# Performance work log

Hardware: AMD Instinct MI355X
Metric: run time of the kernel (lower is better)

Reference implementation:

```python
import jax, jax.numpy as jnp
import numpy as np

N = 100000
E = 1600000
D_IN = 256
N_HEADS = 4
OUT_SZ = 32  # output_dim // n_heads = 128 // 4
ALPHA = 0.2  # leaky relu slope


def setup_inputs() -> dict:
    key = jax.random.key(0)
    ks = jax.random.split(key, 8)
    x = jax.random.normal(ks[0], (N, D_IN), dtype=jnp.float32)
    edge_row = jax.random.randint(ks[1], (E,), 0, N, dtype=jnp.int32)
    edge_col = jax.random.randint(ks[2], (E,), 0, N, dtype=jnp.int32)
    # per-head params: W (conv1d k=1, no bias), a1/a2 (conv1d k=1 with bias)
    W = jax.random.normal(ks[3], (N_HEADS, D_IN, OUT_SZ), dtype=jnp.float32) * (1.0 / np.sqrt(D_IN))
    a1 = jax.random.normal(ks[4], (N_HEADS, OUT_SZ), dtype=jnp.float32) * (1.0 / np.sqrt(OUT_SZ))
    b1 = jnp.zeros((N_HEADS,), dtype=jnp.float32)
    a2 = jax.random.normal(ks[5], (N_HEADS, OUT_SZ), dtype=jnp.float32) * (1.0 / np.sqrt(OUT_SZ))
    b2 = jnp.zeros((N_HEADS,), dtype=jnp.float32)
    return {"x": x, "W": W, "a1": a1, "b1": b1, "a2": a2, "b2": b2,
            "edge_row": edge_row, "edge_col": edge_col}


def _gat_heads(x, W, a1, b1, a2, b2, edge_row, edge_col):
    # per-head linear transform: [H, N, O]
    fts = jnp.einsum('nd,hdo->hno', x, W)
    f1 = jnp.einsum('hno,ho->hn', fts, a1) + b1[:, None]  # [H, N]
    f2 = jnp.einsum('hno,ho->hn', fts, a2) + b2[:, None]  # [H, N]
    # edge logits: f1[row] + f2[col]  (adj values are 1)
    logits = f1[:, edge_row] + f2[:, edge_col]            # [H, E]
    lr = jnp.maximum(ALPHA * logits, logits)
    # segment softmax over each node's incoming edge set (rows)
    seg_max = jax.vmap(lambda v: jax.ops.segment_max(v, edge_row, num_segments=N))(lr)
    ex = jnp.exp(lr - seg_max[:, edge_row])
    denom = jax.vmap(lambda v: jax.ops.segment_sum(v, edge_row, num_segments=N))(ex)
    coef = ex / denom[:, edge_row]                        # [H, E]
    # SpMM aggregation: out[h, i] = sum_{e: row(e)=i} coef[h,e] * fts[h, col(e)]
    msg = coef[:, :, None] * fts[:, edge_col, :]          # [H, E, O]
    agg = jax.vmap(lambda m: jax.ops.segment_sum(m, edge_row, num_segments=N))(msg)  # [H, N, O]
    h = jnp.transpose(agg, (1, 0, 2)).reshape(N, N_HEADS * OUT_SZ)  # concat heads
    return jax.nn.elu(h)[None]  # [1, N, output_dim]


def reference(x, W, a1, b1, a2, b2, edge_row, edge_col):
    return _gat_heads(x, W, a1, b1, a2, b2, edge_row, edge_col)
```

## Files before the change

### kernel.cpp

```cpp
#include <hip/hip_runtime.h>
#include <hip/hip_bf16.h>
#include <math.h>

#define ALPHA 0.2f
#define PB_EDGES 4096
#define MAXT 256

typedef __attribute__((ext_vector_type(8))) short short8;
typedef __attribute__((ext_vector_type(4))) float floatx4;

__device__ __forceinline__ ushort f2bf(float f) {
    uint u = __float_as_uint(f);
    u += 0x7fff + ((u >> 16) & 1);
    return (ushort)(u >> 16);
}

__device__ __forceinline__ short8 pack8(float4 lo, float4 hi) {
    short8 r;
    r[0] = (short)f2bf(lo.x); r[1] = (short)f2bf(lo.y);
    r[2] = (short)f2bf(lo.z); r[3] = (short)f2bf(lo.w);
    r[4] = (short)f2bf(hi.x); r[5] = (short)f2bf(hi.y);
    r[6] = (short)f2bf(hi.z); r[7] = (short)f2bf(hi.w);
    return r;
}

__global__ __launch_bounds__(256) void k_wprep(const float* __restrict__ W,
                                               ushort* __restrict__ Wt)
{
    int g = blockIdx.x * 256 + threadIdx.x;
    int c = g >> 8, d = g & 255;
    Wt[g] = f2bf(W[(c >> 5) * 8192 + d * 32 + (c & 31)]);
}

__global__ __launch_bounds__(256) void k_gemm(const float* __restrict__ x,
                                              const ushort* __restrict__ Wt,
                                              const float* __restrict__ a1v,
                                              const float* __restrict__ b1v,
                                              const float* __restrict__ a2v,
                                              const float* __restrict__ b2v,
                                              ushort* __restrict__ fts2,
                                              float* __restrict__ f1,
                                              float* __restrict__ f2, int M)
{
    __shared__ __align__(16) ushort smem[32768];
    const int t  = threadIdx.x;
    const int m0 = blockIdx.x * 128;

#pragma unroll
    for (int i = 0; i < 16; i++) {
        int f = i * 256 + t;
        int lane_ = f & 63, ksct = f >> 6;
        int ks = ksct & 7, ct = ksct >> 3;
        int mm = lane_ & 15, qq = lane_ >> 4;
        *(uint4*)&smem[f * 8] = *(const uint4*)&Wt[(ct * 16 + mm) * 256 + ks * 32 + qq * 8];
    }

    const int w = t >> 6, lane = t & 63;
    const int mm = lane & 15, qq = lane >> 4;

    int row0 = m0 + w * 32 + mm;
    int row1 = row0 + 16;
    int r0c = (row0 < M) ? row0 : (M - 1);
    int r1c = (row1 < M) ? row1 : (M - 1);
    const float* ar0 = x + (size_t)r0c * 256 + qq * 8;
    const float* ar1 = x + (size_t)r1c * 256 + qq * 8;
    short8 afrag[2][8];
#pragma unroll
    for (int ks = 0; ks < 8; ks++) {
        float4 lo0 = *(const float4*)(ar0 + ks * 32);
        float4 hi0 = *(const float4*)(ar0 + ks * 32 + 4);
        float4 lo1 = *(const float4*)(ar1 + ks * 32);
        float4 hi1 = *(const float4*)(ar1 + ks * 32 + 4);
        afrag[0][ks] = pack8(lo0, hi0);
        afrag[1][ks] = pack8(lo1, hi1);
    }

    floatx4 acc[2][8];
#pragma unroll
    for (int r = 0; r < 2; r++)
#pragma unroll
        for (int ct = 0; ct < 8; ct++) acc[r][ct] = (floatx4){0.f, 0.f, 0.f, 0.f};

    __syncthreads();

#pragma unroll
    for (int ks = 0; ks < 8; ks++) {
#pragma unroll
        for (int ct = 0; ct < 8; ct++) {
            short8 b8 = *(const short8*)&smem[((ct * 8 + ks) * 64 + lane) * 8];
            acc[0][ct] = __builtin_amdgcn_mfma_f32_16x16x32_bf16(afrag[0][ks], b8, acc[0][ct], 0, 0, 0);
            acc[1][ct] = __builtin_amdgcn_mfma_f32_16x16x32_bf16(afrag[1][ks], b8, acc[1][ct], 0, 0, 0);
        }
    }

    __syncthreads();
    ushort* ftsL = smem;
#pragma unroll
    for (int r = 0; r < 2; r++)
#pragma unroll
        for (int ct = 0; ct < 8; ct++)
#pragma unroll
            for (int i = 0; i < 4; i++) {
                int rowl = w * 32 + r * 16 + qq * 4 + i;
                ftsL[rowl * 136 + ct * 16 + mm] = f2bf(acc[r][ct][i]);
            }
    __syncthreads();

    {
        int rowl = t >> 1, half = t & 1;
        int gr = m0 + rowl;
        if (gr < M) {
            const uint4* src = (const uint4*)&ftsL[rowl * 136 + half * 64];
            uint4* dst = (uint4*)(fts2 + (size_t)gr * 128 + half * 64);
#pragma unroll
            for (int i = 0; i < 8; i++) dst[i] = src[i];
        }
    }
#pragma unroll
    for (int p = 0; p < 2; p++) {
        int task = p * 256 + t;
        int rowl = task >> 2, h = task & 3;
        int gr = m0 + rowl;
        if (gr < M) {
            const ushort* fr = &ftsL[rowl * 136 + h * 32];
            float s1 = 0.f, s2 = 0.f;
#pragma unroll
            for (int o = 0; o < 32; o++) {
                float v = __uint_as_float((uint)fr[o] << 16);
                s1 = fmaf(v, a1v[h * 32 + o], s1);
                s2 = fmaf(v, a2v[h * 32 + o], s2);
            }
            f1[gr * 4 + h] = s1 + b1v[h];
            f2[gr * 4 + h] = s2 + b2v[h];
        }
    }
}

__global__ __launch_bounds__(256) void k_phist(const int* __restrict__ erow,
                                               int* __restrict__ bcnt, int E, int NB)
{
    __shared__ int h[512];
    for (int i = threadIdx.x; i < 512; i += 256) h[i] = 0;
    __syncthreads();
    int b0 = blockIdx.x * PB_EDGES;
    int bend = b0 + PB_EDGES; if (bend > E) bend = E;
    for (int j = b0 + threadIdx.x; j < bend; j += 256)
        atomicAdd(&h[erow[j] >> 8], 1);
    __syncthreads();
    for (int i = threadIdx.x; i < NB; i += 256)
        if (h[i]) atomicAdd(&bcnt[i], h[i]);
}

__global__ __launch_bounds__(256) void k_scan_buckets(const int* __restrict__ bcnt,
                                                      int* __restrict__ base,
                                                      int* __restrict__ bcursor,
                                                      int NB, int E)
{
    __shared__ int s[256];
    int t = threadIdx.x;
    int i0 = 2 * t, i1 = 2 * t + 1;
    int v0 = (i0 < NB) ? bcnt[i0] : 0;
    int v1 = (i1 < NB) ? bcnt[i1] : 0;
    int tsum = v0 + v1;
    s[t] = tsum;
    __syncthreads();
    for (int off = 1; off < 256; off <<= 1) {
        int u = (t >= off) ? s[t - off] : 0;
        __syncthreads();
        s[t] += u;
        __syncthreads();
    }
    int excl = s[t] - tsum;
    if (i0 < NB) { base[i0] = excl;      bcursor[i0] = excl; }
    if (i1 < NB) { base[i1] = excl + v0; bcursor[i1] = excl + v0; }
    if (t == 0) base[NB] = E;
}

__global__ __launch_bounds__(256) void k_pscatter(const int* __restrict__ erow,
                                                  const int* __restrict__ ecol,
                                                  int* __restrict__ bcursor,
                                                  uint* __restrict__ part, int E)
{
    __shared__ int h[512];
    __shared__ int cur[512];
    for (int i = threadIdx.x; i < 512; i += 256) h[i] = 0;
    __syncthreads();
    int b0 = blockIdx.x * PB_EDGES;
    int bend = b0 + PB_EDGES; if (bend > E) bend = E;
    for (int j = b0 + threadIdx.x; j < bend; j += 256)
        atomicAdd(&h[erow[j] >> 8], 1);
    __syncthreads();
    for (int i = threadIdx.x; i < 512; i += 256)
        cur[i] = h[i] ? atomicAdd(&bcursor[i], h[i]) : 0;
    __syncthreads();
    for (int j = b0 + threadIdx.x; j < bend; j += 256) {
        int r = erow[j], c = ecol[j];
        int p = atomicAdd(&cur[r >> 8], 1);
        part[p] = ((uint)(r & 255) << 24) | (uint)c;
    }
}

__global__ __launch_bounds__(256) void k_bucket(const uint* __restrict__ part,
                                                const int* __restrict__ base,
                                                int* __restrict__ row_start,
                                                int* __restrict__ col_sorted,
                                                int Nn, int NB, int E)
{
    __shared__ int cnt[256];
    __shared__ int s[256];
    __shared__ int cur[256];
    const int b = blockIdx.x, t = threadIdx.x;
    const int start = base[b], end = base[b + 1];

    cnt[t] = 0;
    __syncthreads();
    for (int j = start + t; j < end; j += 256)
        atomicAdd(&cnt[part[j] >> 24], 1);
    __syncthreads();
    int v = cnt[t];
    s[t] = v;
    __syncthreads();
    for (int off = 1; off < 256; off <<= 1) {
        int u = (t >= off) ? s[t - off] : 0;
        __syncthreads();
        s[t] += u;
        __syncthreads();
    }
    int excl = s[t] - v;
    int r = b * 256 + t;
    if (r < Nn) row_start[r] = start + excl;
    if (b == 0 && t == 0) row_start[Nn] = E;
    cur[t] = start + excl;
    __syncthreads();
    for (int j = start + t; j < end; j += 256) {
        uint rc = part[j];
        int p = atomicAdd(&cur[rc >> 24], 1);
        col_sorted[p] = (int)(rc & 0xffffffu);
    }
}

__global__ __launch_bounds__(256) void k_gat_row(const ushort* __restrict__ fts2,
                                                 const float4* __restrict__ f1,
                                                 const float4* __restrict__ f2,
                                                 const int* __restrict__ row_start,
                                                 const int* __restrict__ cols,
                                                 float* __restrict__ out, int Nn)
{
    __shared__ __align__(16) float eLs[4][MAXT * 4];
    __shared__ uint vLs[4][MAXT];

    const int wid  = threadIdx.x >> 6;
    const int lane = threadIdx.x & 63;
    const int slot = lane >> 4;
    const int sub  = lane & 15;
    const int hsel = sub >> 2;

    const int rbase = (blockIdx.x * 4 + wid) * 4;
    if (rbase >= Nn) return;

    const int myr = rbase + slot;
    const bool rowAct = (myr < Nn);
    const int i0 = rowAct ? myr : Nn;
    const int i1 = (myr + 1 < Nn) ? (myr + 1) : Nn;
    const int sB = row_start[i0];
    const int eB = row_start[i1];
    const int degTot = eB - sB;

    const int s0 = __shfl(sB, 0, 64);
    const int b1 = __shfl(sB, 16, 64);
    const int b2 = __shfl(sB, 32, 64);
    const int b3 = __shfl(sB, 48, 64);
    const int T  = __shfl(eB, 48, 64) - s0;

    float ds = 0.f;
    float acc[8];
#pragma unroll
    for (int i = 0; i < 8; i++) acc[i] = 0.f;

    const char* ftsB = (const char*)fts2;
    const uint  laneOff = (uint)sub * 16;
    float* eLw = eLs[wid];
    uint*  vLw = vLs[wid];

    for (int base = 0; base < T; base += MAXT) {
        int tc = T - base; if (tc > MAXT) tc = MAXT;
        int tcPad = (tc + 63) & ~63;

        for (int lt = lane; lt < tcPad; lt += 64) {
            bool act = (lt < tc);
            int j = s0 + base + lt;
            int c = act ? cols[j] : 0;
            int rsel = (j >= b1) + (j >= b2) + (j >= b3);
            int fi = rbase + rsel; if (fi >= Nn) fi = Nn - 1;
            float4 f1r = f1[fi];
            float4 f2v = f2[c];
            float l0 = f1r.x + f2v.x; l0 = fmaxf(l0, ALPHA * l0);
            float l1 = f1r.y + f2v.y; l1 = fmaxf(l1, ALPHA * l1);
            float l2 = f1r.z + f2v.z; l2 = fmaxf(l2, ALPHA * l2);
            float l3 = f1r.w + f2v.w; l3 = fmaxf(l3, ALPHA * l3);
            float e0 = act ? __expf(l0) : 0.f;
            float e1 = act ? __expf(l1) : 0.f;
            float e2 = act ? __expf(l2) : 0.f;
            float e3 = act ? __expf(l3) : 0.f;
            asm volatile("s_waitcnt lgkmcnt(0)" ::: "memory");
            *(float4*)&eLw[lt * 4] = make_float4(e0, e1, e2, e3);
            vLw[lt] = (uint)c << 8;
        }
        asm volatile("s_waitcnt lgkmcnt(0)" ::: "memory");

        int lo = sB - s0 - base; lo = (lo < 0) ? 0 : ((lo > tc) ? tc : lo);
        int hi = eB - s0 - base; hi = (hi < 0) ? 0 : ((hi > tc) ? tc : hi);
        int ni = hi - lo;
        int eIdx = lo * 4 + hsel;
#pragma unroll 4
        for (int g = 0; g < ni; g++) {
            float ee = eLw[eIdx + g * 4];
            uint  vo = vLw[lo + g] + laneOff;
            uint4 vv = *(const uint4*)(ftsB + vo);
            ds += ee;
            float ve;
            ve = __uint_as_float(vv.x << 16);          acc[0] = fmaf(ee, ve, acc[0]);
            ve = __uint_as_float(vv.x & 0xffff0000u);  acc[1] = fmaf(ee, ve, acc[1]);
            ve = __uint_as_float(vv.y << 16);          acc[2] = fmaf(ee, ve, acc[2]);
            ve = __uint_as_float(vv.y & 0xffff0000u);  acc[3] = fmaf(ee, ve, acc[3]);
            ve = __uint_as_float(vv.z << 16);          acc[4] = fmaf(ee, ve, acc[4]);
            ve = __uint_as_float(vv.z & 0xffff0000u);  acc[5] = fmaf(ee, ve, acc[5]);
            ve = __uint_as_float(vv.w << 16);          acc[6] = fmaf(ee, ve, acc[6]);
            ve = __uint_as_float(vv.w & 0xffff0000u);  acc[7] = fmaf(ee, ve, acc[7]);
        }
    }

    float dsel = (degTot > 0) ? ds : 1.f;
    float rinv = 1.0f / dsel;
    float o[8];
#pragma unroll
    for (int i = 0; i < 8; i++) {
        float v = acc[i] * rinv;
        o[i] = (v > 0.f) ? v : (__expf(v) - 1.0f);
    }
    if (rowAct) {
        float4* dst = (float4*)(out + (size_t)myr * 128 + sub * 8);
        dst[0] = make_float4(o[0], o[1], o[2], o[3]);
        dst[1] = make_float4(o[4], o[5], o[6], o[7]);
    }
}

extern "C" void kernel_launch(void* const* d_in, const int* in_sizes, int n_in,
                              void* d_out, int out_size, void* d_ws, size_t ws_size,
                              hipStream_t stream)
{
    const float* x   = (const float*)d_in[0];
    const float* W   = (const float*)d_in[1];
    const float* a1  = (const float*)d_in[2];
    const float* b1  = (const float*)d_in[3];
    const float* a2  = (const float*)d_in[4];
    const float* b2  = (const float*)d_in[5];
    const int*   erow = (const int*)d_in[6];
    const int*   ecol = (const int*)d_in[7];
    float* out = (float*)d_out;

    const int N = in_sizes[0] / 256;
    const int E = in_sizes[6];
    const int NB = (N + 255) >> 8;

    char*  ws  = (char*)d_ws;
    size_t off = 0;
    auto carve = [&](size_t bytes) -> char* {
        char* p = ws + off;
        off += (bytes + 255) & ~(size_t)255;
        return p;
    };
    ushort* fts2      = (ushort*)carve((size_t)N * 128 * 2);
    ushort* Wt        = (ushort*)carve((size_t)128 * 256 * 2);
    float*  f1        = (float*)carve((size_t)N * 4 * 4);
    float*  f2        = (float*)carve((size_t)N * 4 * 4);
    int*    row_start = (int*)carve(((size_t)N + 1) * 4);
    int*    bcnt      = (int*)carve(512 * 4);
    int*    base      = (int*)carve(513 * 4);
    int*    bcursor   = (int*)carve(512 * 4);
    int*    col_sorted= (int*)carve((size_t)E * 4);
    uint*   part      = (uint*)carve((size_t)E * 4);
    (void)ws_size;

    k_wprep<<<128, 256, 0, stream>>>(W, Wt);
    k_gemm<<<(N + 127) / 128, 256, 0, stream>>>(x, Wt, a1, b1, a2, b2, fts2, f1, f2, N);

    hipMemsetAsync(bcnt, 0, 512 * 4, stream);
    int npb = (E + PB_EDGES - 1) / PB_EDGES;
    k_phist<<<npb, 256, 0, stream>>>(erow, bcnt, E, NB);
    k_scan_buckets<<<1, 256, 0, stream>>>(bcnt, base, bcursor, NB, E);
    k_pscatter<<<npb, 256, 0, stream>>>(erow, ecol, bcursor, part, E);
    k_bucket<<<NB, 256, 0, stream>>>(part, base, row_start, col_sorted, N, NB, E);

    k_gat_row<<<(N + 15) / 16, 256, 0, stream>>>(fts2, (const float4*)f1, (const float4*)f2,
                                                 row_start, col_sorted, out, N);
}
```

Baseline: 337.3 us.

## Software-pipeline SpMM gathers with dual accumulators; read pre-swizzled W directly in GEMM

The aggregation loop now processes two edges per iteration into separate accumulators and prefetches the next pair's feature gathers and weights before doing the current FMAs. This hides gather latency and breaks the dependency chain on one accumulator. The weight prep kernel now writes W in the MFMA fragment layout, so the GEMM loads B fragments straight from global/L2 and no longer stages W in shared memory, which drops two barriers and a 64KB LDS buffer. MAXT is halved to shrink the per-wave LDS staging chunks. Register pressure goes up and the edge staging loop runs more iterations.

```diff
diff --git a/kernel.cpp b/kernel.cpp
--- a/kernel.cpp
+++ b/kernel.cpp
@@ -4,7 +4,7 @@
 
 #define ALPHA 0.2f
 #define PB_EDGES 4096
-#define MAXT 256
+#define MAXT 128
 
 typedef __attribute__((ext_vector_type(8))) short short8;
 typedef __attribute__((ext_vector_type(4))) float floatx4;
@@ -24,11 +24,28 @@
     return r;
 }
 
+__device__ __forceinline__ void fma8(float* acc, float e, uint4 v) {
+    acc[0] = fmaf(e, __uint_as_float(v.x << 16),         acc[0]);
+    acc[1] = fmaf(e, __uint_as_float(v.x & 0xffff0000u), acc[1]);
+    acc[2] = fmaf(e, __uint_as_float(v.y << 16),         acc[2]);
+    acc[3] = fmaf(e, __uint_as_float(v.y & 0xffff0000u), acc[3]);
+    acc[4] = fmaf(e, __uint_as_float(v.z << 16),         acc[4]);
+    acc[5] = fmaf(e, __uint_as_float(v.z & 0xffff0000u), acc[5]);
+    acc[6] = fmaf(e, __uint_as_float(v.w << 16),         acc[6]);
+    acc[7] = fmaf(e, __uint_as_float(v.w & 0xffff0000u), acc[7]);
+}
+
 __global__ __launch_bounds__(256) void k_wprep(const float* __restrict__ W,
                                                ushort* __restrict__ Wt)
 {
     int g = blockIdx.x * 256 + threadIdx.x;
-    int c = g >> 8, d = g & 255;
+    int u = g & 7;
+    int lane = (g >> 3) & 63;
+    int ksct = g >> 9;
+    int ks = ksct & 7, ct = ksct >> 3;
+    int mm = lane & 15, qq = lane >> 4;
+    int c = ct * 16 + mm;
+    int d = ks * 32 + qq * 8 + u;
     Wt[g] = f2bf(W[(c >> 5) * 8192 + d * 32 + (c & 31)]);
 }
 
@@ -42,18 +59,9 @@
                                               float* __restrict__ f1,
                                               float* __restrict__ f2, int M)
 {
-    __shared__ __align__(16) ushort smem[32768];
+    __shared__ __align__(16) ushort ftsL[128 * 136];
     const int t  = threadIdx.x;
     const int m0 = blockIdx.x * 128;
-
-#pragma unroll
-    for (int i = 0; i < 16; i++) {
-        int f = i * 256 + t;
-        int lane_ = f & 63, ksct = f >> 6;
-        int ks = ksct & 7, ct = ksct >> 3;
-        int mm = lane_ & 15, qq = lane_ >> 4;
-        *(uint4*)&smem[f * 8] = *(const uint4*)&Wt[(ct * 16 + mm) * 256 + ks * 32 + qq * 8];
-    }
 
     const int w = t >> 6, lane = t & 63;
     const int mm = lane & 15, qq = lane >> 4;
@@ -81,20 +89,17 @@
 #pragma unroll
         for (int ct = 0; ct < 8; ct++) acc[r][ct] = (floatx4){0.f, 0.f, 0.f, 0.f};
 
-    __syncthreads();
-
+    const ushort* Wf = Wt + (size_t)lane * 8;
 #pragma unroll
     for (int ks = 0; ks < 8; ks++) {
 #pragma unroll
         for (int ct = 0; ct < 8; ct++) {
-            short8 b8 = *(const short8*)&smem[((ct * 8 + ks) * 64 + lane) * 8];
+            short8 b8 = *(const short8*)&Wf[(ct * 8 + ks) * 64 * 8];
             acc[0][ct] = __builtin_amdgcn_mfma_f32_16x16x32_bf16(afrag[0][ks], b8, acc[0][ct], 0, 0, 0);
             acc[1][ct] = __builtin_amdgcn_mfma_f32_16x16x32_bf16(afrag[1][ks], b8, acc[1][ct], 0, 0, 0);
         }
     }
 
-    __syncthreads();
-    ushort* ftsL = smem;
 #pragma unroll
     for (int r = 0; r < 2; r++)
 #pragma unroll
@@ -272,10 +277,10 @@
     const int b3 = __shfl(sB, 48, 64);
     const int T  = __shfl(eB, 48, 64) - s0;
 
-    float ds = 0.f;
-    float acc[8];
-#pragma unroll
-    for (int i = 0; i < 8; i++) acc[i] = 0.f;
+    float dsA = 0.f, dsB = 0.f;
+    float accA[8], accB[8];
+#pragma unroll
+    for (int i = 0; i < 8; i++) { accA[i] = 0.f; accB[i] = 0.f; }
 
     const char* ftsB = (const char*)fts2;
     const uint  laneOff = (uint)sub * 16;
@@ -310,32 +315,48 @@
 
         int lo = sB - s0 - base; lo = (lo < 0) ? 0 : ((lo > tc) ? tc : lo);
         int hi = eB - s0 - base; hi = (hi < 0) ? 0 : ((hi > tc) ? tc : hi);
-        int ni = hi - lo;
-        int eIdx = lo * 4 + hsel;
-#pragma unroll 4
-        for (int g = 0; g < ni; g++) {
-            float ee = eLw[eIdx + g * 4];
-            uint  vo = vLw[lo + g] + laneOff;
-            uint4 vv = *(const uint4*)(ftsB + vo);
-            ds += ee;
-            float ve;
-            ve = __uint_as_float(vv.x << 16);          acc[0] = fmaf(ee, ve, acc[0]);
-            ve = __uint_as_float(vv.x & 0xffff0000u);  acc[1] = fmaf(ee, ve, acc[1]);
-            ve = __uint_as_float(vv.y << 16);          acc[2] = fmaf(ee, ve, acc[2]);
-            ve = __uint_as_float(vv.y & 0xffff0000u);  acc[3] = fmaf(ee, ve, acc[3]);
-            ve = __uint_as_float(vv.z << 16);          acc[4] = fmaf(ee, ve, acc[4]);
-            ve = __uint_as_float(vv.z & 0xffff0000u);  acc[5] = fmaf(ee, ve, acc[5]);
-            ve = __uint_as_float(vv.w << 16);          acc[6] = fmaf(ee, ve, acc[6]);
-            ve = __uint_as_float(vv.w & 0xffff0000u);  acc[7] = fmaf(ee, ve, acc[7]);
-        }
-    }
-
+        int g = lo;
+
+        float eA0 = 0.f, eB0 = 0.f;
+        uint4 vA0 = make_uint4(0, 0, 0, 0), vB0 = make_uint4(0, 0, 0, 0);
+        if (g + 1 < hi) {
+            eA0 = eLw[g * 4 + hsel];
+            eB0 = eLw[g * 4 + 4 + hsel];
+            vA0 = *(const uint4*)(ftsB + (vLw[g] + laneOff));
+            vB0 = *(const uint4*)(ftsB + (vLw[g + 1] + laneOff));
+        }
+#pragma unroll 2
+        for (; g + 3 < hi; g += 2) {
+            float eA1 = eLw[(g + 2) * 4 + hsel];
+            float eB1 = eLw[(g + 2) * 4 + 4 + hsel];
+            uint4 vA1 = *(const uint4*)(ftsB + (vLw[g + 2] + laneOff));
+            uint4 vB1 = *(const uint4*)(ftsB + (vLw[g + 3] + laneOff));
+            dsA += eA0; dsB += eB0;
+            fma8(accA, eA0, vA0);
+            fma8(accB, eB0, vB0);
+            eA0 = eA1; eB0 = eB1; vA0 = vA1; vB0 = vB1;
+        }
+        if (g + 1 < hi) {
+            dsA += eA0; dsB += eB0;
+            fma8(accA, eA0, vA0);
+            fma8(accB, eB0, vB0);
+            g += 2;
+        }
+        if (g < hi) {
+            float eA = eLw[g * 4 + hsel];
+            uint4 vA = *(const uint4*)(ftsB + (vLw[g] + laneOff));
+            dsA += eA;
+            fma8(accA, eA, vA);
+        }
+    }
+
+    float ds = dsA + dsB;
     float dsel = (degTot > 0) ? ds : 1.f;
     float rinv = 1.0f / dsel;
     float o[8];
 #pragma unroll
     for (int i = 0; i < 8; i++) {
-        float v = acc[i] * rinv;
+        float v = (accA[i] + accB[i]) * rinv;
         o[i] = (v > 0.f) ? v : (__expf(v) - 1.0f);
     }
     if (rowAct) {
```

Result: no change. 334.7 us (-0.8%).
